# Optimization experiments

Measured on AMD Instinct MI355X. Metric: run time of the kernel, lower is better.

Reference implementation:

```python
import jax, jax.numpy as jnp
import numpy as np

L, D, N_HEADS = 4096, 1024, 16
HEAD_D = D // N_HEADS


def setup_inputs() -> dict:
    key = jax.random.key(0)
    kx, kq, kbq, ko, kbo = jax.random.split(key, 5)
    lim_in = 1.0 / np.sqrt(D)
    return {
        "x": jax.random.normal(kx, (L, D), dtype=jnp.float32),
        # equinox nn.Linear(dim, 3*dim): weight [3D, D], bias [3D], uniform(-1/sqrt(in), 1/sqrt(in))
        "W_qkv": jax.random.uniform(kq, (3 * D, D), jnp.float32, -lim_in, lim_in),
        "b_qkv": jax.random.uniform(kbq, (3 * D,), jnp.float32, -lim_in, lim_in),
        "W_out": jax.random.uniform(ko, (D, D), jnp.float32, -lim_in, lim_in),
        "b_out": jax.random.uniform(kbo, (D,), jnp.float32, -lim_in, lim_in),
    }


def reference(x, W_qkv, b_qkv, W_out, b_out):
    # qkv projection: equinox Linear computes W @ x + b per token -> x @ W.T + b
    qkv = x @ W_qkv.T + b_qkv                         # [L, 3D]
    qkv = qkv.reshape(L, 3, N_HEADS, HEAD_D)
    qkv = jnp.transpose(qkv, (1, 2, 0, 3))            # [3, n, L, d]
    q, k, v = qkv[0], qkv[1], qkv[2]                  # each [n, L, d]

    scale = 1.0 / jnp.sqrt(jnp.asarray(HEAD_D, dtype=x.dtype))
    attn = jnp.einsum('nqd,nkd->nqk', q, k) * scale   # [n, L, L]
    causal = jnp.tril(jnp.ones((L, L), dtype=bool))
    attn = jnp.where(causal, attn, -jnp.inf)
    attn = jax.nn.softmax(attn, axis=-1)              # dropout rate 0 -> identity
    out = jnp.einsum('nqk,nkd->nqd', attn, v)         # [n, L, d]
    out = jnp.transpose(out, (1, 0, 2)).reshape(L, D)
    return out @ W_out.T + b_out                      # [L, D]
```

## Files before the change

kernel.cpp:

```cpp
#include <hip/hip_runtime.h>
#include <hip/hip_bf16.h>
#include <math.h>

#define L_SEQ 4096
#define DIM   1024
#define NH    16
#define HD    64

#define QSCL 0.18033688011112042f

typedef __attribute__((ext_vector_type(4)))  float f32x4;
typedef __attribute__((ext_vector_type(16))) float f32x16;
typedef __attribute__((ext_vector_type(8)))  short s16x8;
typedef __attribute__((ext_vector_type(4)))  short s16x4;
typedef __attribute__((ext_vector_type(4)))  unsigned u32x4;
typedef __attribute__((ext_vector_type(2)))  unsigned u32x2;

#if defined(__has_builtin)
#  if __has_builtin(__builtin_amdgcn_permlane32_swap)
#    define HAVE_PLSWAP 1
#  else
#    define HAVE_PLSWAP 0
#  endif
#else
#  define HAVE_PLSWAP 0
#endif

__device__ __forceinline__ short f2bf(float f) {
  unsigned u = __builtin_bit_cast(unsigned, f);
  u = u + 0x7fffu + ((u >> 16) & 1u);
  return (short)(u >> 16);
}

__device__ __forceinline__ unsigned cvt_pk_bf16(float lo, float hi_) {
  unsigned r;
  asm("v_cvt_pk_bf16_f32 %0, %1, %2" : "=v"(r) : "v"(lo), "v"(hi_));
  return r;
}

__device__ __forceinline__ float exp2_fast(float x) {
  float r;
  asm("v_exp_f32 %0, %1" : "=v"(r) : "v"(x));
  return r;
}

__device__ __forceinline__ void gload_lds16(const void* g, void* l) {
  __builtin_amdgcn_global_load_lds(
      (__attribute__((address_space(1))) void*)(g),
      (__attribute__((address_space(3))) void*)(l), 16, 0, 0);
}

#define CVT_N1 (L_SEQ * DIM / 4)
#define CVT_N2 (3 * DIM * DIM / 4)
#define CVT_N3 (DIM * DIM / 4)

__global__ __launch_bounds__(256) void cvt_all(const float* __restrict__ x,
                                               const float* __restrict__ Wqkv,
                                               const float* __restrict__ Wout,
                                               short* __restrict__ xb,
                                               short* __restrict__ wqkvb,
                                               short* __restrict__ woutb) {
  int i = blockIdx.x * 256 + threadIdx.x;
  const float* src;
  short* dst;
  int j;
  if (i < CVT_N1)               { src = x;    dst = xb;    j = i; }
  else if (i < CVT_N1 + CVT_N2) { src = Wqkv; dst = wqkvb; j = i - CVT_N1; }
  else                          { src = Wout; dst = woutb; j = i - CVT_N1 - CVT_N2; }
  f32x4 f = *(const f32x4*)(src + j * 4);
  s16x4 o;
  o[0] = f2bf(f[0]); o[1] = f2bf(f[1]); o[2] = f2bf(f[2]); o[3] = f2bf(f[3]);
  *(s16x4*)(dst + j * 4) = o;
}

__global__ __launch_bounds__(256) void gemm_qkv64(const short* __restrict__ A,
                                                  const short* __restrict__ B,
                                                  const float* __restrict__ bias,
                                                  short* __restrict__ Qb,
                                                  short* __restrict__ Kf,
                                                  short* __restrict__ Vf) {
  __shared__ __align__(16) short As[64 * 32];
  __shared__ __align__(16) short Bs[128 * 32];
  const int t = threadIdx.x;
  const int w = t >> 6, l = t & 63;
  const int lr = l & 15, lg = l >> 4;
  const int bid = blockIdx.x;
  const int xcd = bid & 7;
  const int ii = bid >> 3;
  const int bm = xcd * 8 + (ii & 7);
  const int bn = ii >> 3;
  const bool isV = (bn >= 16);

  f32x4 acc[4][2];
#pragma unroll
  for (int m = 0; m < 4; ++m)
#pragma unroll
    for (int n = 0; n < 2; ++n) acc[m][n] = (f32x4)0.f;

  const short* aptr = A + (bm * 64 + w * 16 + (l >> 2)) * DIM + (l & 3) * 8;
  const short* bptr = B + (bn * 128 + w * 16 + (l >> 2)) * DIM + (l & 3) * 8;
  short* asl = &As[(w * 16) * 32];
  short* bsl = &Bs[(w * 16) * 32];

  for (int kk = 0; kk < DIM; kk += 32) {
    gload_lds16(aptr + kk, asl);
    gload_lds16(bptr + kk, bsl);
    gload_lds16(bptr + kk + 64 * DIM, bsl + 64 * 32);
    __syncthreads();
    s16x8 af[4], bfr[2];
#pragma unroll
    for (int m = 0; m < 4; ++m)
      af[m] = *(const s16x8*)&As[(m * 16 + lr) * 32 + lg * 8];
#pragma unroll
    for (int n = 0; n < 2; ++n)
      bfr[n] = *(const s16x8*)&Bs[(w * 32 + n * 16 + lr) * 32 + lg * 8];
    if (isV) {
#pragma unroll
      for (int m = 0; m < 4; ++m)
#pragma unroll
        for (int n = 0; n < 2; ++n)
          acc[m][n] = __builtin_amdgcn_mfma_f32_16x16x32_bf16(af[m], bfr[n], acc[m][n], 0, 0, 0);
    } else {
#pragma unroll
      for (int m = 0; m < 4; ++m)
#pragma unroll
        for (int n = 0; n < 2; ++n)
          acc[m][n] = __builtin_amdgcn_mfma_f32_16x16x32_bf16(bfr[n], af[m], acc[m][n], 0, 0, 0);
    }
    __syncthreads();
  }

  if (!isV) {
    const int row0x = bm * 64;
#pragma unroll
    for (int n = 0; n < 2; ++n) {
      const int colb = bn * 128 + w * 32 + n * 16 + lg * 4;
      const f32x4 bv4 = *(const f32x4*)&bias[colb];
      const int which = colb >> 10;
      const int head = (colb & 1023) >> 6;
      const int d0 = colb & 63;
      if (which == 0) {
        short* dst = Qb + head * (L_SEQ * HD);
#pragma unroll
        for (int m = 0; m < 4; ++m) {
          const int xrow = row0x + m * 16 + lr;
          s16x4 wv;
#pragma unroll
          for (int j = 0; j < 4; ++j) wv[j] = f2bf((acc[m][n][j] + bv4[j]) * QSCL);
          *(s16x4*)&dst[xrow * HD + d0] = wv;
        }
      } else {
        short* dst = Kf + head * (L_SEQ * HD);
        const int c = d0 >> 4, khi = (d0 >> 3) & 1, e0 = d0 & 7;
#pragma unroll
        for (int m = 0; m < 4; ++m) {
          const int xrow = row0x + m * 16 + lr;
          const int p = xrow >> 5;
          const int lane = khi * 32 + (xrow & 31);
          s16x4 wv;
#pragma unroll
          for (int j = 0; j < 4; ++j) wv[j] = f2bf(acc[m][n][j] + bv4[j]);
          *(s16x4*)&dst[((p * 4 + c) * 64 + lane) * 8 + e0] = wv;
        }
      }
    }
  } else {
#pragma unroll
    for (int n = 0; n < 2; ++n) {
      const int col = bn * 128 + w * 32 + n * 16 + lr;
      const float bv = bias[col];
      const int head = (col & 1023) >> 6;
      const int d = col & 63;
      const int dh = d >> 5;
      const int dq = d & 31;
      short* dst = Vf + head * (L_SEQ * HD);
#pragma unroll
      for (int m = 0; m < 4; ++m) {
        const int rowb = bm * 64 + m * 16 + lg * 4;
        const int tt = rowb >> 6;
        const int kc = (rowb >> 4) & 3;
        const int khi = (rowb >> 3) & 1;
        const int e0 = rowb & 7;
        s16x4 wv;
#pragma unroll
        for (int j = 0; j < 4; ++j) wv[j] = f2bf(acc[m][n][j] + bv);
        *(s16x4*)&dst[(((tt * 4 + kc) * 2 + dh) * 64 + khi * 32 + dq) * 8 + e0] = wv;
      }
    }
  }
}

__global__ __launch_bounds__(256) void gemm_out64(const short* __restrict__ A,
                                                  const short* __restrict__ B,
                                                  const float* __restrict__ bias,
                                                  float* __restrict__ C) {
  __shared__ __align__(16) short As[64 * 32];
  __shared__ __align__(16) short Bs[64 * 32];
  const int t = threadIdx.x;
  const int w = t >> 6, l = t & 63;
  const int wr = w >> 1, wc = w & 1;
  const int lr = l & 15, lg = l >> 4;
  const int bid = blockIdx.x;
  const int xcd = bid & 7;
  const int ii = bid >> 3;
  const int bm = xcd * 8 + (ii & 7);
  const int bn = ii >> 3;

  f32x4 acc[2][2];
#pragma unroll
  for (int m = 0; m < 2; ++m)
#pragma unroll
    for (int n = 0; n < 2; ++n) acc[m][n] = (f32x4)0.f;

  const short* aptr = A + (bm * 64 + (t >> 2)) * DIM + (t & 3) * 8;
  const short* bptr = B + (bn * 64 + (t >> 2)) * DIM + (t & 3) * 8;
  short* asl = &As[t * 8];
  short* bsl = &Bs[t * 8];

  for (int kk = 0; kk < DIM; kk += 32) {
    gload_lds16(aptr + kk, asl);
    gload_lds16(bptr + kk, bsl);
    __syncthreads();
    s16x8 af[2], bfr[2];
#pragma unroll
    for (int m = 0; m < 2; ++m)
      af[m] = *(const s16x8*)&As[(wr * 32 + m * 16 + lr) * 32 + lg * 8];
#pragma unroll
    for (int n = 0; n < 2; ++n)
      bfr[n] = *(const s16x8*)&Bs[(wc * 32 + n * 16 + lr) * 32 + lg * 8];
#pragma unroll
    for (int m = 0; m < 2; ++m)
#pragma unroll
      for (int n = 0; n < 2; ++n)
        acc[m][n] = __builtin_amdgcn_mfma_f32_16x16x32_bf16(af[m], bfr[n], acc[m][n], 0, 0, 0);
    __syncthreads();
  }

  const int row0 = bm * 64 + wr * 32;
  const int col0 = bn * 64 + wc * 32;
#pragma unroll
  for (int n = 0; n < 2; ++n) {
    const int col = col0 + n * 16 + lr;
    const float bv = bias[col];
#pragma unroll
    for (int m = 0; m < 2; ++m)
#pragma unroll
      for (int j = 0; j < 4; ++j) {
        const int row = row0 + m * 16 + lg * 4 + j;
        C[row * DIM + col] = acc[m][n][j] + bv;
      }
  }
}

__global__ __launch_bounds__(256, 4) void attn64(const short* __restrict__ Qb,
                                                 const short* __restrict__ Kf,
                                                 const short* __restrict__ Vf,
                                                 short* __restrict__ Ob) {
  __shared__ __align__(16) short KV[2][8192];
  const int bid = blockIdx.x;
  const int xcd = bid & 7;
  const int i = bid >> 3;
  const int head = (xcd << 1) | (i >> 6);
  const int j = i & 63;
  const int qt = (j < 32) ? (63 - j) : (j - 32);
  const int q0 = qt * 64;
  const int h = threadIdx.x >> 6;
  const int l = threadIdx.x & 63;
  const int q = l & 31;
  const int hi = l >> 5;
  const int sb = h >> 1;
  const int p = h & 1;

  const short* Qh = Qb + head * (L_SEQ * HD);
  const short* Kh = Kf + head * (L_SEQ * HD);
  const short* Vh = Vf + head * (L_SEQ * HD);
  const short* gKV = (h < 2) ? Kh : Vh;

  s16x8 qf[4];
#pragma unroll
  for (int c = 0; c < 4; ++c)
    qf[c] = *(const s16x8*)&Qh[(q0 + sb * 32 + q) * HD + c * 16 + hi * 8];

  f32x16 o0 = (f32x16)0.f, o1 = (f32x16)0.f;
  f32x4 lvec = (f32x4)0.f;

  const int nr = qt + 1;

  {
    const short* gsrc = gKV + p * 2048;
    short* lb = &KV[0][h * 2048];
#pragma unroll
    for (int c = 0; c < 4; ++c) gload_lds16(gsrc + c * 512 + l * 8, lb + c * 512);
  }
  __syncthreads();

  for (int r = 0; r < nr; ++r) {
    const int buf = r & 1;
    if (r + 1 < nr) {
      const short* gsrc = gKV + (2 * (r + 1) + p) * 2048;
      short* lb = &KV[buf ^ 1][h * 2048];
#pragma unroll
      for (int c = 0; c < 4; ++c) gload_lds16(gsrc + c * 512 + l * 8, lb + c * 512);
    }

    const bool last = (r == nr - 1);
    if (!(h == 1 && last)) {
      const short* kb = &KV[buf][p * 2048];
      const short* vb = &KV[buf][(2 + p) * 2048];

      s16x8 kfr[4];
#pragma unroll
      for (int c = 0; c < 4; ++c)
        kfr[c] = *(const s16x8*)&kb[c * 512 + l * 8];

      f32x16 s = (f32x16)0.f;
      __builtin_amdgcn_s_setprio(1);
#pragma unroll
      for (int c = 0; c < 4; ++c)
        s = __builtin_amdgcn_mfma_f32_32x32x16_bf16(kfr[c], qf[c], s, 0, 0, 0);
      __builtin_amdgcn_s_setprio(0);

      if (last && (h == 0 || h == 3)) {
        const int qrel = q - hi * 4;
#pragma unroll
        for (int rr = 0; rr < 16; ++rr) {
          const int koff = (rr & 3) + 8 * (rr >> 2);
          if (koff > qrel) s[rr] = -1e30f;
        }
      }

#pragma unroll
      for (int rr = 0; rr < 16; ++rr) s[rr] = exp2_fast(s[rr]);
#pragma unroll
      for (int rr = 0; rr < 16; ++rr) lvec[rr & 3] += s[rr];

#pragma unroll
      for (int cc = 0; cc < 2; ++cc) {
        const int roff = cc * 8;
        const unsigned A = cvt_pk_bf16(s[roff + 0], s[roff + 1]);
        const unsigned B = cvt_pk_bf16(s[roff + 2], s[roff + 3]);
        const unsigned C = cvt_pk_bf16(s[roff + 4], s[roff + 5]);
        const unsigned D = cvt_pk_bf16(s[roff + 6], s[roff + 7]);
        u32x4 pw;
#if HAVE_PLSWAP
        const u32x2 r02 = __builtin_amdgcn_permlane32_swap(A, C, false, false);
        const u32x2 r13 = __builtin_amdgcn_permlane32_swap(B, D, false, false);
        pw[0] = r02[0]; pw[1] = r13[0]; pw[2] = r02[1]; pw[3] = r13[1];
#else
        const unsigned sA = (unsigned)__shfl_xor((int)A, 32, 64);
        const unsigned sB = (unsigned)__shfl_xor((int)B, 32, 64);
        const unsigned sC = (unsigned)__shfl_xor((int)C, 32, 64);
        const unsigned sD = (unsigned)__shfl_xor((int)D, 32, 64);
        pw[0] = hi ? sC : A; pw[1] = hi ? sD : B;
        pw[2] = hi ? C : sA; pw[3] = hi ? D : sB;
#endif
        const s16x8 pf = __builtin_bit_cast(s16x8, pw);
        const s16x8 vf0 = *(const s16x8*)&vb[(cc * 2 + 0) * 512 + l * 8];
        const s16x8 vf1 = *(const s16x8*)&vb[(cc * 2 + 1) * 512 + l * 8];
        __builtin_amdgcn_s_setprio(1);
        o0 = __builtin_amdgcn_mfma_f32_32x32x16_bf16(vf0, pf, o0, 0, 0, 0);
        o1 = __builtin_amdgcn_mfma_f32_32x32x16_bf16(vf1, pf, o1, 0, 0, 0);
        __builtin_amdgcn_s_setprio(0);
      }
    }
    __syncthreads();
  }

  float lsum = (lvec[0] + lvec[1]) + (lvec[2] + lvec[3]);
  lsum += __shfl_xor(lsum, 32, 64);

  unsigned* Ms = (unsigned*)&KV[0][0];
  if (p == 1) {
    unsigned* st = Ms + (sb * 64 + l) * 17;
#pragma unroll
    for (int w2 = 0; w2 < 8; ++w2) st[w2]     = cvt_pk_bf16(o0[2 * w2], o0[2 * w2 + 1]);
#pragma unroll
    for (int w2 = 0; w2 < 8; ++w2) st[8 + w2] = cvt_pk_bf16(o1[2 * w2], o1[2 * w2 + 1]);
    st[16] = __builtin_bit_cast(unsigned, lsum);
  }
  __syncthreads();
  if (p == 0) {
    const unsigned* st = Ms + (sb * 64 + l) * 17;
    lsum += __builtin_bit_cast(float, st[16]);
#pragma unroll
    for (int w2 = 0; w2 < 8; ++w2) {
      const unsigned ua = st[w2];
      o0[2 * w2]     += __builtin_bit_cast(float, ua << 16);
      o0[2 * w2 + 1] += __builtin_bit_cast(float, ua & 0xffff0000u);
      const unsigned ub = st[8 + w2];
      o1[2 * w2]     += __builtin_bit_cast(float, ub << 16);
      o1[2 * w2 + 1] += __builtin_bit_cast(float, ub & 0xffff0000u);
    }
    const float inv = 1.f / lsum;
    const int orow = q0 + sb * 32 + q;
#pragma unroll
    for (int dh = 0; dh < 2; ++dh) {
#pragma unroll
      for (int tq = 0; tq < 4; ++tq) {
        s16x4 wv;
#pragma unroll
        for (int jj = 0; jj < 4; ++jj) {
          const int rr = tq * 4 + jj;
          const float ov = (dh == 0) ? o0[rr] : o1[rr];
          wv[jj] = f2bf(ov * inv);
        }
        *(s16x4*)&Ob[orow * DIM + head * HD + dh * 32 + tq * 8 + hi * 4] = wv;
      }
    }
  }
}

extern "C" void kernel_launch(void* const* d_in, const int* in_sizes, int n_in,
                              void* d_out, int out_size, void* d_ws, size_t ws_size,
                              hipStream_t stream) {
  const float* x    = (const float*)d_in[0];
  const float* Wqkv = (const float*)d_in[1];
  const float* bqkv = (const float*)d_in[2];
  const float* Wout = (const float*)d_in[3];
  const float* bout = (const float*)d_in[4];
  float* out = (float*)d_out;

  char* ws = (char*)d_ws;
  short* xb    = (short*)(ws);
  short* wqkvb = (short*)(ws + (8u  << 20));
  short* woutb = (short*)(ws + (14u << 20));
  short* Qb    = (short*)(ws + (16u << 20));
  short* Kf    = (short*)(ws + (24u << 20));
  short* Vf    = (short*)(ws + (32u << 20));
  short* Ob    = (short*)(ws + (40u << 20));

  cvt_all<<<(CVT_N1 + CVT_N2 + CVT_N3) / 256, 256, 0, stream>>>(x, Wqkv, Wout, xb, wqkvb, woutb);

  gemm_qkv64<<<1536, 256, 0, stream>>>(xb, wqkvb, bqkv, Qb, Kf, Vf);
  attn64<<<1024, 256, 0, stream>>>(Qb, Kf, Vf, Ob);
  gemm_out64<<<1024, 256, 0, stream>>>(Ob, woutb, bout, out);
}
```

Baseline: 123.7 us.

## Fuse fp32-to-bf16 conversion of x and Wqkv into QKV GEMM loads

The QKV GEMM now reads fp32 x and Wqkv straight from global memory, converts them to bf16 in registers with packed cvt instructions, and writes them to LDS. This removes the separate conversion pass over those tensors and its bf16 round trip through memory, leaving a standalone conversion only for Wout. In exchange, the GEMM reads twice as many bytes per tile, and the direct global-to-LDS async loads become synchronous register loads, which can stall the MFMA loop. Separately, the attention QK^T MFMA chain is split into two independent accumulators to shorten the dependency chain.

```diff
diff --git a/kernel.cpp b/kernel.cpp
--- a/kernel.cpp
+++ b/kernel.cpp
@@ -38,6 +38,15 @@
   return r;
 }
 
+__device__ __forceinline__ s16x8 cvt8(const f32x4 a, const f32x4 b) {
+  u32x4 u;
+  u[0] = cvt_pk_bf16(a[0], a[1]);
+  u[1] = cvt_pk_bf16(a[2], a[3]);
+  u[2] = cvt_pk_bf16(b[0], b[1]);
+  u[3] = cvt_pk_bf16(b[2], b[3]);
+  return __builtin_bit_cast(s16x8, u);
+}
+
 __device__ __forceinline__ float exp2_fast(float x) {
   float r;
   asm("v_exp_f32 %0, %1" : "=v"(r) : "v"(x));
@@ -50,31 +59,19 @@
       (__attribute__((address_space(3))) void*)(l), 16, 0, 0);
 }
 
-#define CVT_N1 (L_SEQ * DIM / 4)
-#define CVT_N2 (3 * DIM * DIM / 4)
 #define CVT_N3 (DIM * DIM / 4)
 
-__global__ __launch_bounds__(256) void cvt_all(const float* __restrict__ x,
-                                               const float* __restrict__ Wqkv,
-                                               const float* __restrict__ Wout,
-                                               short* __restrict__ xb,
-                                               short* __restrict__ wqkvb,
-                                               short* __restrict__ woutb) {
+__global__ __launch_bounds__(256) void cvt_wout(const float* __restrict__ Wout,
+                                                short* __restrict__ woutb) {
   int i = blockIdx.x * 256 + threadIdx.x;
-  const float* src;
-  short* dst;
-  int j;
-  if (i < CVT_N1)               { src = x;    dst = xb;    j = i; }
-  else if (i < CVT_N1 + CVT_N2) { src = Wqkv; dst = wqkvb; j = i - CVT_N1; }
-  else                          { src = Wout; dst = woutb; j = i - CVT_N1 - CVT_N2; }
-  f32x4 f = *(const f32x4*)(src + j * 4);
+  f32x4 f = *(const f32x4*)(Wout + i * 4);
   s16x4 o;
   o[0] = f2bf(f[0]); o[1] = f2bf(f[1]); o[2] = f2bf(f[2]); o[3] = f2bf(f[3]);
-  *(s16x4*)(dst + j * 4) = o;
-}
-
-__global__ __launch_bounds__(256) void gemm_qkv64(const short* __restrict__ A,
-                                                  const short* __restrict__ B,
+  *(s16x4*)(woutb + i * 4) = o;
+}
+
+__global__ __launch_bounds__(256) void gemm_qkv64(const float* __restrict__ A,
+                                                  const float* __restrict__ B,
                                                   const float* __restrict__ bias,
                                                   short* __restrict__ Qb,
                                                   short* __restrict__ Kf,
@@ -97,15 +94,22 @@
 #pragma unroll
     for (int n = 0; n < 2; ++n) acc[m][n] = (f32x4)0.f;
 
-  const short* aptr = A + (bm * 64 + w * 16 + (l >> 2)) * DIM + (l & 3) * 8;
-  const short* bptr = B + (bn * 128 + w * 16 + (l >> 2)) * DIM + (l & 3) * 8;
-  short* asl = &As[(w * 16) * 32];
-  short* bsl = &Bs[(w * 16) * 32];
+  const float* ap = A + (bm * 64 + (t >> 2)) * DIM + (t & 3) * 8;
+  const float* bp = B + (bn * 128 + (t >> 2)) * DIM + (t & 3) * 8;
+  short* aw = &As[(t >> 2) * 32 + (t & 3) * 8];
+  short* bw0 = &Bs[(t >> 2) * 32 + (t & 3) * 8];
+  short* bw1 = &Bs[(64 + (t >> 2)) * 32 + (t & 3) * 8];
 
   for (int kk = 0; kk < DIM; kk += 32) {
-    gload_lds16(aptr + kk, asl);
-    gload_lds16(bptr + kk, bsl);
-    gload_lds16(bptr + kk + 64 * DIM, bsl + 64 * 32);
+    const f32x4 a0 = *(const f32x4*)(ap + kk);
+    const f32x4 a1 = *(const f32x4*)(ap + kk + 4);
+    const f32x4 b0 = *(const f32x4*)(bp + kk);
+    const f32x4 b1 = *(const f32x4*)(bp + kk + 4);
+    const f32x4 c0 = *(const f32x4*)(bp + 64 * DIM + kk);
+    const f32x4 c1 = *(const f32x4*)(bp + 64 * DIM + kk + 4);
+    *(s16x8*)aw  = cvt8(a0, a1);
+    *(s16x8*)bw0 = cvt8(b0, b1);
+    *(s16x8*)bw1 = cvt8(c0, c1);
     __syncthreads();
     s16x8 af[4], bfr[2];
 #pragma unroll
@@ -313,12 +317,15 @@
       for (int c = 0; c < 4; ++c)
         kfr[c] = *(const s16x8*)&kb[c * 512 + l * 8];
 
-      f32x16 s = (f32x16)0.f;
+      f32x16 s = (f32x16)0.f, s2 = (f32x16)0.f;
       __builtin_amdgcn_s_setprio(1);
-#pragma unroll
-      for (int c = 0; c < 4; ++c)
-        s = __builtin_amdgcn_mfma_f32_32x32x16_bf16(kfr[c], qf[c], s, 0, 0, 0);
+      s  = __builtin_amdgcn_mfma_f32_32x32x16_bf16(kfr[0], qf[0], s,  0, 0, 0);
+      s2 = __builtin_amdgcn_mfma_f32_32x32x16_bf16(kfr[2], qf[2], s2, 0, 0, 0);
+      s  = __builtin_amdgcn_mfma_f32_32x32x16_bf16(kfr[1], qf[1], s,  0, 0, 0);
+      s2 = __builtin_amdgcn_mfma_f32_32x32x16_bf16(kfr[3], qf[3], s2, 0, 0, 0);
       __builtin_amdgcn_s_setprio(0);
+#pragma unroll
+      for (int rr = 0; rr < 16; ++rr) s[rr] += s2[rr];
 
       if (last && (h == 0 || h == 3)) {
         const int qrel = q - hi * 4;
@@ -421,17 +428,15 @@
   float* out = (float*)d_out;
 
   char* ws = (char*)d_ws;
-  short* xb    = (short*)(ws);
-  short* wqkvb = (short*)(ws + (8u  << 20));
   short* woutb = (short*)(ws + (14u << 20));
   short* Qb    = (short*)(ws + (16u << 20));
   short* Kf    = (short*)(ws + (24u << 20));
   short* Vf    = (short*)(ws + (32u << 20));
   short* Ob    = (short*)(ws + (40u << 20));
 
-  cvt_all<<<(CVT_N1 + CVT_N2 + CVT_N3) / 256, 256, 0, stream>>>(x, Wqkv, Wout, xb, wqkvb, woutb);
-
-  gemm_qkv64<<<1536, 256, 0, stream>>>(xb, wqkvb, bqkv, Qb, Kf, Vf);
+  cvt_wout<<<CVT_N3 / 256, 256, 0, stream>>>(Wout, woutb);
+
+  gemm_qkv64<<<1536, 256, 0, stream>>>(x, Wqkv, bqkv, Qb, Kf, Vf);
   attn64<<<1024, 256, 0, stream>>>(Qb, Kf, Vf, Ob);
   gemm_out64<<<1024, 256, 0, stream>>>(Ob, woutb, bout, out);
 }
```

Result: slower. 137.5 us (+11.1%).

## Triple-buffer K/V tiles in attention with prefetch distance two

Applied to the files above, without the earlier changes.

Grows the LDS K/V staging from two buffers to three and issues global-to-LDS loads two iterations ahead instead of one. Full __syncthreads is replaced by explicit vmcnt waits that drain only the older load batch, followed by a raw s_barrier. The aim is to hide more global-memory latency behind the MFMA work. In exchange LDS use per block rises to 48 KB, which may cut occupancy below the 4 blocks requested by launch bounds, and the hand-written vmcnt counts must stay correct.

```diff
diff --git a/kernel.cpp b/kernel.cpp
--- a/kernel.cpp
+++ b/kernel.cpp
@@ -256,7 +256,7 @@
                                                  const short* __restrict__ Kf,
                                                  const short* __restrict__ Vf,
                                                  short* __restrict__ Ob) {
-  __shared__ __align__(16) short KV[2][8192];
+  __shared__ __align__(16) short KV[3][8192];
   const int bid = blockIdx.x;
   const int xcd = bid & 7;
   const int i = bid >> 3;
@@ -287,26 +287,37 @@
   const int nr = qt + 1;
 
   {
-    const short* gsrc = gKV + p * 2048;
-    short* lb = &KV[0][h * 2048];
-#pragma unroll
-    for (int c = 0; c < 4; ++c) gload_lds16(gsrc + c * 512 + l * 8, lb + c * 512);
-  }
-  __syncthreads();
-
+    const short* g0 = gKV + p * 2048;
+    short* lb0 = &KV[0][h * 2048];
+#pragma unroll
+    for (int c = 0; c < 4; ++c) gload_lds16(g0 + c * 512 + l * 8, lb0 + c * 512);
+    if (nr > 1) {
+      const short* g1 = gKV + (2 + p) * 2048;
+      short* lb1 = &KV[1][h * 2048];
+#pragma unroll
+      for (int c = 0; c < 4; ++c) gload_lds16(g1 + c * 512 + l * 8, lb1 + c * 512);
+      asm volatile("s_waitcnt vmcnt(4)" ::: "memory");
+    } else {
+      asm volatile("s_waitcnt vmcnt(0)" ::: "memory");
+    }
+  }
+  __builtin_amdgcn_s_barrier();
+
+  int cur = 0;
   for (int r = 0; r < nr; ++r) {
-    const int buf = r & 1;
-    if (r + 1 < nr) {
-      const short* gsrc = gKV + (2 * (r + 1) + p) * 2048;
-      short* lb = &KV[buf ^ 1][h * 2048];
+    const bool staged = (r + 2 < nr);
+    if (staged) {
+      const int nx2 = (cur + 2 >= 3) ? (cur - 1) : (cur + 2);
+      const short* gsrc = gKV + (2 * (r + 2) + p) * 2048;
+      short* lb = &KV[nx2][h * 2048];
 #pragma unroll
       for (int c = 0; c < 4; ++c) gload_lds16(gsrc + c * 512 + l * 8, lb + c * 512);
     }
 
     const bool last = (r == nr - 1);
     if (!(h == 1 && last)) {
-      const short* kb = &KV[buf][p * 2048];
-      const short* vb = &KV[buf][(2 + p) * 2048];
+      const short* kb = &KV[cur][p * 2048];
+      const short* vb = &KV[cur][(2 + p) * 2048];
 
       s16x8 kfr[4];
 #pragma unroll
@@ -363,7 +374,11 @@
         __builtin_amdgcn_s_setprio(0);
       }
     }
-    __syncthreads();
+
+    if (staged) asm volatile("s_waitcnt vmcnt(4)" ::: "memory");
+    else        asm volatile("s_waitcnt vmcnt(0)" ::: "memory");
+    __builtin_amdgcn_s_barrier();
+    cur = (cur + 1 == 3) ? 0 : cur + 1;
   }
 
   float lsum = (lvec[0] + lvec[1]) + (lvec[2] + lvec[3]);
```

Result: slower. 132.6 us (+7.2%).
